# Optimization experiments

Measured on AMD Instinct MI355X. Metric: run time of the kernel, lower is better.

## Reference

```python
import jax, jax.numpy as jnp
import numpy as np

B, H, S, D = 2, 16, 2048, 64  # batch, heads, seq (n_qry == n_tok), head_dim


def setup_inputs() -> dict:
    key = jax.random.key(0)
    kq, kk, kv = jax.random.split(key, 3)
    Q = jax.random.normal(kq, (B, H, S, D), dtype=jnp.float32)
    K_cache = jax.random.normal(kk, (B, H, S, D), dtype=jnp.float32)
    V_cache = jax.random.normal(kv, (B, H, S, D), dtype=jnp.float32)
    return {"Q": Q, "K_cache": K_cache, "V_cache": V_cache}


def reference(Q, K_cache, V_cache):
    n_qry = Q.shape[-2]
    n_tok = K_cache.shape[-2]
    scale = 1.0 / jnp.sqrt(jnp.asarray(Q.shape[-1], Q.dtype))
    # [B, H, n_qry, n_tok] scores
    A = jnp.einsum('bhqd,bhkd->bhqk', Q, K_cache) * scale
    # causal mask: query q may attend key k iff k <= q + (n_tok - n_qry)
    q_idx = jnp.arange(n_qry)[:, None]
    k_idx = jnp.arange(n_tok)[None, :]
    mask = k_idx <= q_idx + (n_tok - n_qry)
    A = jnp.where(mask, A, -jnp.inf)
    P = jax.nn.softmax(A, axis=-1)
    return jnp.einsum('bhqk,bhkd->bhqd', P, V_cache)
```

## Files before the change

kernel.cpp:

```cpp
#include <hip/hip_runtime.h>

typedef __attribute__((ext_vector_type(8))) short bf16x8;
typedef __attribute__((ext_vector_type(4))) float f32x4;

#define NB 2
#define NH 16
#define NS 2048
#define ND 64
#define NBH 32
#define QSCALE (0.125f * 1.44269504088896f)
#define CMAX 12.0f

static __device__ __forceinline__ unsigned pack2(float lo, float hi) {
  return __builtin_amdgcn_perm(__builtin_bit_cast(unsigned, hi),
                               __builtin_bit_cast(unsigned, lo), 0x07060302u);
}


__global__ __launch_bounds__(256) void prep_kernel(const float* __restrict__ K,
                                                   const float* __restrict__ V,
                                                   short* __restrict__ W) {
  const int xcd = blockIdx.x & 7;
  const int rest = blockIdx.x >> 3;
  const int lb = rest >> 5;
  const int kb = rest & 31;
  const int bh = xcd * 4 + lb;
  const float* Kp = K + (size_t)bh * NS * ND + (size_t)kb * 64 * ND;
  const float* Vp = V + (size_t)bh * NS * ND + (size_t)kb * 64 * ND;
  short* Wp = W + ((size_t)bh * 32 + kb) * 8192;

  __shared__ float vt[64 * 65];

  {
    int vrow = threadIdx.x >> 2, seg = threadIdx.x & 3;
    const float* src = Vp + vrow * ND + seg * 16;
    float* dst = vt + vrow * 65 + seg * 16;
#pragma unroll
    for (int i = 0; i < 4; ++i) {
      float4 v = *(const float4*)(src + i * 4);
      dst[i * 4 + 0] = v.x; dst[i * 4 + 1] = v.y;
      dst[i * 4 + 2] = v.z; dst[i * 4 + 3] = v.w;
    }
  }

#pragma unroll
  for (int e0 = 0; e0 < 512; e0 += 256) {
    int e = e0 + threadIdx.x;
    int c = e >> 6, lane = e & 63;
    int st = c >> 1, cc = c & 1, quad = lane >> 4, col = lane & 15;
    int prow = 32 * (st >> 1) + 8 * (col >> 2) + 4 * (st & 1) + (col & 3);
    const float* kr = Kp + prow * ND + cc * 32 + quad * 8;
    float4 a = *(const float4*)kr;
    float4 b = *(const float4*)(kr + 4);
    uint4 u = {pack2(a.x, a.y), pack2(a.z, a.w), pack2(b.x, b.y), pack2(b.z, b.w)};
    *(uint4*)(Wp + (size_t)e * 8) = u;
  }
  __syncthreads();

#pragma unroll
  for (int e0 = 0; e0 < 512; e0 += 256) {
    int e = e0 + threadIdx.x;
    int c = e >> 6, lane = e & 63;
    int g = c >> 2, t = c & 3, quad = lane >> 4, col = lane & 15;
    const float* base = vt + (32 * g + 8 * quad) * 65 + t * 16 + col;
    float f[8];
#pragma unroll
    for (int j = 0; j < 8; ++j) f[j] = base[j * 65];
    uint4 u = {pack2(f[0], f[1]), pack2(f[2], f[3]),
               pack2(f[4], f[5]), pack2(f[6], f[7])};
    *(uint4*)(Wp + 4096 + (size_t)e * 8) = u;
  }
}

__global__ __launch_bounds__(256, 2) void fa_kernel(
    const float* __restrict__ Q, const short* __restrict__ W,
    float* __restrict__ O) {
  const int lane = threadIdx.x & 63;
  const int wave = threadIdx.x >> 6;
  const int col  = lane & 15;
  const int quad = lane >> 4;

  const int i = blockIdx.x;
  const int xcd = i & 7;
  const int j = i >> 3;
  const int phase = j >> 5;
  const int slot = j & 31;
  const int bh = xcd * 4 + (slot & 3);
  const int rblk = slot >> 2;
  const int r = phase ? (15 - rblk) : rblk;
  const int qg = r * 4 + wave;
  const int T = (qg >> 1) + 1;

  const float* Qp = Q + (size_t)bh * NS * ND;
  const short* Wb = W + (size_t)bh * 32 * 8192;
  float*       Op = O + (size_t)bh * NS * ND;

  bf16x8 qf[2][2];
#pragma unroll
  for (int f = 0; f < 2; ++f) {
    const float* qrow = Qp + (size_t)(qg * 32 + f * 16 + col) * ND + quad * 8;
#pragma unroll
    for (int c = 0; c < 2; ++c) {
      float4 a = *(const float4*)(qrow + c * 32);
      float4 b = *(const float4*)(qrow + c * 32 + 4);
      union { bf16x8 v; unsigned u[4]; } t;
      t.u[0] = pack2(a.x * QSCALE, a.y * QSCALE);
      t.u[1] = pack2(a.z * QSCALE, a.w * QSCALE);
      t.u[2] = pack2(b.x * QSCALE, b.y * QSCALE);
      t.u[3] = pack2(b.z * QSCALE, b.w * QSCALE);
      qf[f][c] = t.v;
    }
  }

  f32x4 o4[2][4];
#pragma unroll
  for (int f = 0; f < 2; ++f)
#pragma unroll
    for (int t = 0; t < 4; ++t) o4[f][t] = (f32x4){0.f, 0.f, 0.f, 0.f};
  float lsum[2] = {0.f, 0.f};

  auto computeTile = [&](const bf16x8 (&kf)[8], const bf16x8 (&vf)[8],
                         bool last) {
    float sc[2][4][4];
#pragma unroll
    for (int st = 0; st < 4; ++st) {
#pragma unroll
      for (int f = 0; f < 2; ++f) {
        f32x4 acc = (f32x4){-CMAX, -CMAX, -CMAX, -CMAX};
        acc = __builtin_amdgcn_mfma_f32_16x16x32_bf16(kf[st * 2 + 0], qf[f][0],
                                                      acc, 0, 0, 0);
        acc = __builtin_amdgcn_mfma_f32_16x16x32_bf16(kf[st * 2 + 1], qf[f][1],
                                                      acc, 0, 0, 0);
#pragma unroll
        for (int rr = 0; rr < 4; ++rr) sc[f][st][rr] = acc[rr];
      }
    }

    if (last) {
#pragma unroll
      for (int f = 0; f < 2; ++f) {
        int qrel = (qg & 1) * 32 + f * 16 + col;
#pragma unroll
        for (int st = 0; st < 4; ++st)
#pragma unroll
          for (int rr = 0; rr < 4; ++rr) {
            int phys = 32 * (st >> 1) + 8 * quad + 4 * (st & 1) + rr;
            if (phys > qrel) sc[f][st][rr] = -INFINITY;
          }
      }
    }

    bf16x8 pf[2][2];
#pragma unroll
    for (int f = 0; f < 2; ++f)
#pragma unroll
      for (int g = 0; g < 2; ++g) {
        float p0 = __builtin_amdgcn_exp2f(sc[f][2 * g + 0][0]);
        float p1 = __builtin_amdgcn_exp2f(sc[f][2 * g + 0][1]);
        float p2 = __builtin_amdgcn_exp2f(sc[f][2 * g + 0][2]);
        float p3 = __builtin_amdgcn_exp2f(sc[f][2 * g + 0][3]);
        float p4 = __builtin_amdgcn_exp2f(sc[f][2 * g + 1][0]);
        float p5 = __builtin_amdgcn_exp2f(sc[f][2 * g + 1][1]);
        float p6 = __builtin_amdgcn_exp2f(sc[f][2 * g + 1][2]);
        float p7 = __builtin_amdgcn_exp2f(sc[f][2 * g + 1][3]);
        lsum[f] += ((p0 + p1) + (p2 + p3)) + ((p4 + p5) + (p6 + p7));
        union { bf16x8 v; unsigned u[4]; } tt;
        tt.u[0] = pack2(p0, p1);
        tt.u[1] = pack2(p2, p3);
        tt.u[2] = pack2(p4, p5);
        tt.u[3] = pack2(p6, p7);
        pf[f][g] = tt.v;
      }

#pragma unroll
    for (int g = 0; g < 2; ++g)
#pragma unroll
      for (int t4 = 0; t4 < 4; ++t4) {
#pragma unroll
        for (int f = 0; f < 2; ++f)
          o4[f][t4] = __builtin_amdgcn_mfma_f32_16x16x32_bf16(
              pf[f][g], vf[g * 4 + t4], o4[f][t4], 0, 0, 0);
      }
  };

  bf16x8 ka[8], kb[8], va[8], vb[8];
#pragma unroll
  for (int c = 0; c < 8; ++c) {
    ka[c] = *(const bf16x8*)(Wb + c * 512 + lane * 8);
    va[c] = *(const bf16x8*)(Wb + 4096 + c * 512 + lane * 8);
  }

  for (int t = 0; t < T; t += 2) {
    const short* b1 = Wb + (size_t)(t + 1) * 8192;
    if (t + 1 < T) {
#pragma unroll
      for (int c = 0; c < 8; ++c) {
        kb[c] = *(const bf16x8*)(b1 + c * 512 + lane * 8);
        vb[c] = *(const bf16x8*)(b1 + 4096 + c * 512 + lane * 8);
      }
    }
    computeTile(ka, va, t == T - 1);
    if (t + 1 < T) {
      if (t + 2 < T) {
        const short* b2 = b1 + 8192;
#pragma unroll
        for (int c = 0; c < 8; ++c) {
          ka[c] = *(const bf16x8*)(b2 + c * 512 + lane * 8);
          va[c] = *(const bf16x8*)(b2 + 4096 + c * 512 + lane * 8);
        }
      }
      computeTile(kb, vb, t + 1 == T - 1);
    }
  }

#pragma unroll
  for (int f = 0; f < 2; ++f) {
    float lt = lsum[f];
    lt += __shfl_xor(lt, 16, 64);
    lt += __shfl_xor(lt, 32, 64);
#pragma unroll
    for (int rr = 0; rr < 4; ++rr) {
      float lr = __shfl(lt, quad * 4 + rr, 64);
      float inv = 1.0f / lr;
      float* orow = Op + (size_t)(qg * 32 + f * 16 + quad * 4 + rr) * ND + col;
#pragma unroll
      for (int t4 = 0; t4 < 4; ++t4) orow[t4 * 16] = o4[f][t4][rr] * inv;
    }
  }
}

extern "C" void kernel_launch(void* const* d_in, const int* in_sizes, int n_in,
                              void* d_out, int out_size, void* d_ws, size_t ws_size,
                              hipStream_t stream) {
  const float* Q = (const float*)d_in[0];
  const float* K = (const float*)d_in[1];
  const float* V = (const float*)d_in[2];
  short* W = (short*)d_ws;
  hipLaunchKernelGGL(prep_kernel, dim3(NBH * 32), dim3(256), 0, stream, K, V, W);
  hipLaunchKernelGGL(fa_kernel, dim3(512), dim3(256), 0, stream, Q, W,
                     (float*)d_out);
}
```

Measured before the change: 118.0 us.

## Fuse K/V bf16 prep into attention kernel via cooperative grid sync

Merges the separate prep kernel into the attention kernel. Each of the 512 blocks converts two K/V tiles to the packed bf16 layout, then all blocks meet at a cooperative grid-wide barrier before running attention. This removes one kernel launch and the gap between the two kernels. In exchange it needs a cooperative launch that fits all 512 blocks at once, and pays for a grid sync. If the cooperative launch fails, it falls back to the old two-kernel path.

```diff
diff --git a/kernel.cpp b/kernel.cpp
--- a/kernel.cpp
+++ b/kernel.cpp
@@ -1,4 +1,7 @@
 #include <hip/hip_runtime.h>
+#include <hip/hip_cooperative_groups.h>
+
+namespace cg = cooperative_groups;
 
 typedef __attribute__((ext_vector_type(8))) short bf16x8;
 typedef __attribute__((ext_vector_type(4))) float f32x4;
@@ -229,6 +232,219 @@
   }
 }
 
+__global__ __launch_bounds__(256, 2) void fa_fused(
+    const float* __restrict__ Q, const float* __restrict__ K,
+    const float* __restrict__ V, short* __restrict__ W,
+    float* __restrict__ O) {
+  const int lane = threadIdx.x & 63;
+  const int wave = threadIdx.x >> 6;
+  const int col  = lane & 15;
+  const int quad = lane >> 4;
+
+  const int i = blockIdx.x;
+  const int xcd = i & 7;
+  const int j = i >> 3;
+  const int phase = j >> 5;
+  const int slot = j & 31;
+  const int bh = xcd * 4 + (slot & 3);
+  const int rblk = slot >> 2;
+  const int r = phase ? (15 - rblk) : rblk;
+  const int qg = r * 4 + wave;
+  const int T = (qg >> 1) + 1;
+
+  const float* Qp = Q + (size_t)bh * NS * ND;
+  short*       Wb = W + (size_t)bh * 32 * 8192;
+  float*       Op = O + (size_t)bh * NS * ND;
+
+  bf16x8 qf[2][2];
+#pragma unroll
+  for (int f = 0; f < 2; ++f) {
+    const float* qrow = Qp + (size_t)(qg * 32 + f * 16 + col) * ND + quad * 8;
+#pragma unroll
+    for (int c = 0; c < 2; ++c) {
+      float4 a = *(const float4*)(qrow + c * 32);
+      float4 b = *(const float4*)(qrow + c * 32 + 4);
+      union { bf16x8 v; unsigned u[4]; } t;
+      t.u[0] = pack2(a.x * QSCALE, a.y * QSCALE);
+      t.u[1] = pack2(a.z * QSCALE, a.w * QSCALE);
+      t.u[2] = pack2(b.x * QSCALE, b.y * QSCALE);
+      t.u[3] = pack2(b.z * QSCALE, b.w * QSCALE);
+      qf[f][c] = t.v;
+    }
+  }
+
+  __shared__ float vt[64 * 65];
+#pragma unroll
+  for (int tt = 0; tt < 2; ++tt) {
+    const int kb = phase * 16 + rblk * 2 + tt;
+    const float* Kp = K + (size_t)bh * NS * ND + (size_t)kb * 64 * ND;
+    const float* Vp = V + (size_t)bh * NS * ND + (size_t)kb * 64 * ND;
+    short* Wp = Wb + (size_t)kb * 8192;
+
+    {
+      int vrow = threadIdx.x >> 2, seg = threadIdx.x & 3;
+      const float* src = Vp + vrow * ND + seg * 16;
+      float* dst = vt + vrow * 65 + seg * 16;
+#pragma unroll
+      for (int ii = 0; ii < 4; ++ii) {
+        float4 v = *(const float4*)(src + ii * 4);
+        dst[ii * 4 + 0] = v.x; dst[ii * 4 + 1] = v.y;
+        dst[ii * 4 + 2] = v.z; dst[ii * 4 + 3] = v.w;
+      }
+    }
+
+#pragma unroll
+    for (int e0 = 0; e0 < 512; e0 += 256) {
+      int e = e0 + threadIdx.x;
+      int c = e >> 6, ln = e & 63;
+      int st = c >> 1, cc = c & 1, qd = ln >> 4, cl = ln & 15;
+      int prow = 32 * (st >> 1) + 8 * (cl >> 2) + 4 * (st & 1) + (cl & 3);
+      const float* kr = Kp + prow * ND + cc * 32 + qd * 8;
+      float4 a = *(const float4*)kr;
+      float4 b = *(const float4*)(kr + 4);
+      uint4 u = {pack2(a.x, a.y), pack2(a.z, a.w), pack2(b.x, b.y), pack2(b.z, b.w)};
+      *(uint4*)(Wp + (size_t)e * 8) = u;
+    }
+    __syncthreads();
+
+#pragma unroll
+    for (int e0 = 0; e0 < 512; e0 += 256) {
+      int e = e0 + threadIdx.x;
+      int c = e >> 6, ln = e & 63;
+      int g = c >> 2, t = c & 3, qd = ln >> 4, cl = ln & 15;
+      const float* base = vt + (32 * g + 8 * qd) * 65 + t * 16 + cl;
+      float f[8];
+#pragma unroll
+      for (int jj = 0; jj < 8; ++jj) f[jj] = base[jj * 65];
+      uint4 u = {pack2(f[0], f[1]), pack2(f[2], f[3]),
+                 pack2(f[4], f[5]), pack2(f[6], f[7])};
+      *(uint4*)(Wp + 4096 + (size_t)e * 8) = u;
+    }
+    __syncthreads();
+  }
+
+  __builtin_amdgcn_fence(__ATOMIC_RELEASE, "agent");
+  cg::this_grid().sync();
+  __builtin_amdgcn_fence(__ATOMIC_ACQUIRE, "agent");
+
+  f32x4 o4[2][4];
+#pragma unroll
+  for (int f = 0; f < 2; ++f)
+#pragma unroll
+    for (int t = 0; t < 4; ++t) o4[f][t] = (f32x4){0.f, 0.f, 0.f, 0.f};
+  float lsum[2] = {0.f, 0.f};
+
+  auto computeTile = [&](const bf16x8 (&kf)[8], const bf16x8 (&vf)[8],
+                         bool last) {
+    float sc[2][4][4];
+#pragma unroll
+    for (int st = 0; st < 4; ++st) {
+#pragma unroll
+      for (int f = 0; f < 2; ++f) {
+        f32x4 acc = (f32x4){-CMAX, -CMAX, -CMAX, -CMAX};
+        acc = __builtin_amdgcn_mfma_f32_16x16x32_bf16(kf[st * 2 + 0], qf[f][0],
+                                                      acc, 0, 0, 0);
+        acc = __builtin_amdgcn_mfma_f32_16x16x32_bf16(kf[st * 2 + 1], qf[f][1],
+                                                      acc, 0, 0, 0);
+#pragma unroll
+        for (int rr = 0; rr < 4; ++rr) sc[f][st][rr] = acc[rr];
+      }
+    }
+
+    if (last) {
+#pragma unroll
+      for (int f = 0; f < 2; ++f) {
+        int qrel = (qg & 1) * 32 + f * 16 + col;
+#pragma unroll
+        for (int st = 0; st < 4; ++st)
+#pragma unroll
+          for (int rr = 0; rr < 4; ++rr) {
+            int phys = 32 * (st >> 1) + 8 * quad + 4 * (st & 1) + rr;
+            if (phys > qrel) sc[f][st][rr] = -INFINITY;
+          }
+      }
+    }
+
+    bf16x8 pf[2][2];
+#pragma unroll
+    for (int f = 0; f < 2; ++f)
+#pragma unroll
+      for (int g = 0; g < 2; ++g) {
+        float p0 = __builtin_amdgcn_exp2f(sc[f][2 * g + 0][0]);
+        float p1 = __builtin_amdgcn_exp2f(sc[f][2 * g + 0][1]);
+        float p2 = __builtin_amdgcn_exp2f(sc[f][2 * g + 0][2]);
+        float p3 = __builtin_amdgcn_exp2f(sc[f][2 * g + 0][3]);
+        float p4 = __builtin_amdgcn_exp2f(sc[f][2 * g + 1][0]);
+        float p5 = __builtin_amdgcn_exp2f(sc[f][2 * g + 1][1]);
+        float p6 = __builtin_amdgcn_exp2f(sc[f][2 * g + 1][2]);
+        float p7 = __builtin_amdgcn_exp2f(sc[f][2 * g + 1][3]);
+        lsum[f] += ((p0 + p1) + (p2 + p3)) + ((p4 + p5) + (p6 + p7));
+        union { bf16x8 v; unsigned u[4]; } tt;
+        tt.u[0] = pack2(p0, p1);
+        tt.u[1] = pack2(p2, p3);
+        tt.u[2] = pack2(p4, p5);
+        tt.u[3] = pack2(p6, p7);
+        pf[f][g] = tt.v;
+      }
+
+#pragma unroll
+    for (int g = 0; g < 2; ++g)
+#pragma unroll
+      for (int t4 = 0; t4 < 4; ++t4) {
+#pragma unroll
+        for (int f = 0; f < 2; ++f)
+          o4[f][t4] = __builtin_amdgcn_mfma_f32_16x16x32_bf16(
+              pf[f][g], vf[g * 4 + t4], o4[f][t4], 0, 0, 0);
+      }
+  };
+
+  const short* Wr = Wb;
+  bf16x8 ka[8], kb2[8], va[8], vb[8];
+#pragma unroll
+  for (int c = 0; c < 8; ++c) {
+    ka[c] = *(const bf16x8*)(Wr + c * 512 + lane * 8);
+    va[c] = *(const bf16x8*)(Wr + 4096 + c * 512 + lane * 8);
+  }
+
+  for (int t = 0; t < T; t += 2) {
+    const short* b1 = Wr + (size_t)(t + 1) * 8192;
+    if (t + 1 < T) {
+#pragma unroll
+      for (int c = 0; c < 8; ++c) {
+        kb2[c] = *(const bf16x8*)(b1 + c * 512 + lane * 8);
+        vb[c] = *(const bf16x8*)(b1 + 4096 + c * 512 + lane * 8);
+      }
+    }
+    computeTile(ka, va, t == T - 1);
+    if (t + 1 < T) {
+      if (t + 2 < T) {
+        const short* b2 = b1 + 8192;
+#pragma unroll
+        for (int c = 0; c < 8; ++c) {
+          ka[c] = *(const bf16x8*)(b2 + c * 512 + lane * 8);
+          va[c] = *(const bf16x8*)(b2 + 4096 + c * 512 + lane * 8);
+        }
+      }
+      computeTile(kb2, vb, t + 1 == T - 1);
+    }
+  }
+
+#pragma unroll
+  for (int f = 0; f < 2; ++f) {
+    float lt = lsum[f];
+    lt += __shfl_xor(lt, 16, 64);
+    lt += __shfl_xor(lt, 32, 64);
+#pragma unroll
+    for (int rr = 0; rr < 4; ++rr) {
+      float lr = __shfl(lt, quad * 4 + rr, 64);
+      float inv = 1.0f / lr;
+      float* orow = Op + (size_t)(qg * 32 + f * 16 + quad * 4 + rr) * ND + col;
+#pragma unroll
+      for (int t4 = 0; t4 < 4; ++t4) orow[t4 * 16] = o4[f][t4][rr] * inv;
+    }
+  }
+}
+
 extern "C" void kernel_launch(void* const* d_in, const int* in_sizes, int n_in,
                               void* d_out, int out_size, void* d_ws, size_t ws_size,
                               hipStream_t stream) {
@@ -236,7 +452,13 @@
   const float* K = (const float*)d_in[1];
   const float* V = (const float*)d_in[2];
   short* W = (short*)d_ws;
-  hipLaunchKernelGGL(prep_kernel, dim3(NBH * 32), dim3(256), 0, stream, K, V, W);
-  hipLaunchKernelGGL(fa_kernel, dim3(512), dim3(256), 0, stream, Q, W,
-                     (float*)d_out);
+  float* O = (float*)d_out;
+
+  void* args[] = {(void*)&Q, (void*)&K, (void*)&V, (void*)&W, (void*)&O};
+  hipError_t e = hipLaunchCooperativeKernel((const void*)fa_fused, dim3(512),
+                                            dim3(256), args, 0, stream);
+  if (e != hipSuccess) {
+    hipLaunchKernelGGL(prep_kernel, dim3(NBH * 32), dim3(256), 0, stream, K, V, W);
+    hipLaunchKernelGGL(fa_kernel, dim3(512), dim3(256), 0, stream, Q, W, O);
+  }
 }
```

Result: slower. 251.1 us (+112.9%).

## Share K/V tiles across waves via LDS with async global_load_lds double buffering

Applied to the files above, without the earlier changes.

Before, each of the four waves loaded every K/V tile from global memory into its own registers. Now the block cooperatively stages each 16 KB tile into a double-buffered LDS array using global_load_lds, and all waves read their fragments from LDS. The aim is to cut redundant global/L2 traffic fourfold and to free the registers that held the prefetched tiles. The cost is a block-wide barrier per tile, 32 KB of LDS per block, and waves with fewer tiles idling until the block's longest wave finishes.

```diff
diff --git a/kernel.cpp b/kernel.cpp
--- a/kernel.cpp
+++ b/kernel.cpp
@@ -14,6 +14,12 @@
 static __device__ __forceinline__ unsigned pack2(float lo, float hi) {
   return __builtin_amdgcn_perm(__builtin_bit_cast(unsigned, hi),
                                __builtin_bit_cast(unsigned, lo), 0x07060302u);
+}
+
+static __device__ __forceinline__ void stage16(const short* g, short* l) {
+  __builtin_amdgcn_global_load_lds(
+      (const __attribute__((address_space(1))) void*)g,
+      (__attribute__((address_space(3))) void*)l, 16, 0, 0);
 }
 
 
@@ -90,10 +96,13 @@
   const int r = phase ? (15 - rblk) : rblk;
   const int qg = r * 4 + wave;
   const int T = (qg >> 1) + 1;
+  const int Tblk = 2 * r + 2;
 
   const float* Qp = Q + (size_t)bh * NS * ND;
   const short* Wb = W + (size_t)bh * 32 * 8192;
   float*       Op = O + (size_t)bh * NS * ND;
+
+  __shared__ short lbuf[2][8192];
 
   bf16x8 qf[2][2];
 #pragma unroll
@@ -119,8 +128,23 @@
     for (int t = 0; t < 4; ++t) o4[f][t] = (f32x4){0.f, 0.f, 0.f, 0.f};
   float lsum[2] = {0.f, 0.f};
 
-  auto computeTile = [&](const bf16x8 (&kf)[8], const bf16x8 (&vf)[8],
-                         bool last) {
+  auto stage = [&](int buf, int t) {
+    const short* src = Wb + (size_t)t * 8192;
+#pragma unroll
+    for (int i2 = 0; i2 < 4; ++i2) {
+      int cc = wave * 4 + i2;
+      stage16(src + cc * 512 + lane * 8, &lbuf[buf][cc * 512]);
+    }
+  };
+
+  auto computeTile = [&](int buf, bool last) {
+    bf16x8 kf[8], vf[8];
+#pragma unroll
+    for (int c = 0; c < 8; ++c) {
+      kf[c] = *(const bf16x8*)(&lbuf[buf][c * 512 + lane * 8]);
+      vf[c] = *(const bf16x8*)(&lbuf[buf][4096 + c * 512 + lane * 8]);
+    }
+
     float sc[2][4][4];
 #pragma unroll
     for (int st = 0; st < 4; ++st) {
@@ -183,34 +207,16 @@
       }
   };
 
-  bf16x8 ka[8], kb[8], va[8], vb[8];
-#pragma unroll
-  for (int c = 0; c < 8; ++c) {
-    ka[c] = *(const bf16x8*)(Wb + c * 512 + lane * 8);
-    va[c] = *(const bf16x8*)(Wb + 4096 + c * 512 + lane * 8);
-  }
-
-  for (int t = 0; t < T; t += 2) {
-    const short* b1 = Wb + (size_t)(t + 1) * 8192;
-    if (t + 1 < T) {
-#pragma unroll
-      for (int c = 0; c < 8; ++c) {
-        kb[c] = *(const bf16x8*)(b1 + c * 512 + lane * 8);
-        vb[c] = *(const bf16x8*)(b1 + 4096 + c * 512 + lane * 8);
-      }
-    }
-    computeTile(ka, va, t == T - 1);
-    if (t + 1 < T) {
-      if (t + 2 < T) {
-        const short* b2 = b1 + 8192;
-#pragma unroll
-        for (int c = 0; c < 8; ++c) {
-          ka[c] = *(const bf16x8*)(b2 + c * 512 + lane * 8);
-          va[c] = *(const bf16x8*)(b2 + 4096 + c * 512 + lane * 8);
-        }
-      }
-      computeTile(kb, vb, t + 1 == T - 1);
-    }
+  stage(0, 0);
+  asm volatile("s_waitcnt vmcnt(0)" ::: "memory");
+  __syncthreads();
+  int cur = 0;
+  for (int t = 0; t < Tblk; ++t) {
+    if (t + 1 < Tblk) stage(cur ^ 1, t + 1);
+    if (t < T) computeTile(cur, t == T - 1);
+    asm volatile("s_waitcnt vmcnt(0)" ::: "memory");
+    __syncthreads();
+    cur ^= 1;
   }
 
 #pragma unroll
```

Measured after the change: 118.6 us. About the same (+0.5%).
